# Performance work log

Hardware: AMD Instinct MI355X
Metric: run time of the kernel (lower is better)

## Reference

```python
import jax, jax.numpy as jnp
import numpy as np

B, S, H = 2, 2048, 3072
NH, NKV, HD = 16, 16, 256
Q_SIZE = NH * HD          # 4096
KV_SIZE = NKV * HD        # 4096
ROPE_THETA = 10000.0


def setup_inputs() -> dict:
    key = jax.random.key(0)
    k1, k2, k3 = jax.random.split(key, 3)
    hidden_states = jax.random.normal(k1, (B, S, H), dtype=jnp.float32)
    positions = jnp.arange(B * S, dtype=jnp.int32).reshape(B, S) % S  # 0..S-1 per row
    Wqkv = jax.random.normal(k2, (H, Q_SIZE + 2 * KV_SIZE), dtype=jnp.float32) * 0.02
    Wo = jax.random.normal(k3, (Q_SIZE, H), dtype=jnp.float32) * 0.02
    return {"hidden_states": hidden_states, "positions": positions, "Wqkv": Wqkv, "Wo": Wo}


def _apply_rope_neox(x, positions, head_dim, theta):
    # x: [B, S, nheads, head_dim]; neox style: rotate halves
    half = head_dim // 2
    inv_freq = 1.0 / (theta ** (jnp.arange(0, head_dim, 2, dtype=jnp.float32) / head_dim))  # [half]
    angles = positions.astype(jnp.float32)[..., None] * inv_freq  # [B, S, half]
    cos = jnp.cos(angles)[:, :, None, :]  # [B, S, 1, half]
    sin = jnp.sin(angles)[:, :, None, :]
    x1, x2 = x[..., :half], x[..., half:]
    return jnp.concatenate([x1 * cos - x2 * sin, x2 * cos + x1 * sin], axis=-1)


def reference(hidden_states, positions, Wqkv, Wo):
    # fused QKV projection (bias-free)
    qkv = jnp.einsum('bsh,hd->bsd', hidden_states, Wqkv)
    q, k, v = jnp.split(qkv, [Q_SIZE, Q_SIZE + KV_SIZE], axis=-1)
    q = q.reshape(B, S, NH, HD)
    k = k.reshape(B, S, NKV, HD)
    v = v.reshape(B, S, NKV, HD)
    # RoPE (neox style, rotary_dim == head_dim)
    q = _apply_rope_neox(q, positions, HD, ROPE_THETA)
    k = _apply_rope_neox(k, positions, HD, ROPE_THETA)
    # GQA: repeat kv heads if fewer than query heads
    if NKV != NH:
        rep = NH // NKV
        k = jnp.repeat(k, rep, axis=2)
        v = jnp.repeat(v, rep, axis=2)
    scale = float(HD) ** -0.5
    scores = jnp.einsum('bqhd,bkhd->bhqk', q, k) * scale  # [B, NH, S, S]
    causal = jnp.tril(jnp.ones((S, S), dtype=bool))
    scores = jnp.where(causal[None, None], scores, jnp.finfo(scores.dtype).min)
    probs = jax.nn.softmax(scores, axis=-1)
    attn = jnp.einsum('bhqk,bkhd->bqhd', probs, v).reshape(B, S, Q_SIZE)
    return jnp.einsum('bsd,dh->bsh', attn, Wo)
```

## Files before the change

### kernel.cpp

```cpp
#include <hip/hip_runtime.h>

#define SQLEN 2048
#define QKVW 12288
#define NHEADS 16
#define HEADD 256

typedef unsigned short u16;
typedef __bf16 bf16x8 __attribute__((ext_vector_type(8)));
typedef float f32x4 __attribute__((ext_vector_type(4)));

__device__ __forceinline__ float bf2f(u16 u) {
  union { unsigned int i; float f; } v; v.i = ((unsigned int)u) << 16; return v.f;
}
__device__ __forceinline__ u16 f2bf(float f) {
  union { float f; unsigned int i; } v; v.f = f;
  unsigned int x = v.i;
  return (u16)((x + 0x7fffu + ((x >> 16) & 1u)) >> 16);
}

__device__ __forceinline__ void gl_lds16(const u16* g, u16* l) {
  __builtin_amdgcn_global_load_lds(
      (const __attribute__((address_space(1))) void*)g,
      (__attribute__((address_space(3))) void*)l, 16, 0, 0);
}

__global__ __launch_bounds__(256) void f32_to_bf16(
    const float* __restrict__ src, u16* __restrict__ dst) {
  long i = (long)(blockIdx.x * 256 + threadIdx.x) * 8;
  float4 a = *reinterpret_cast<const float4*>(src + i);
  float4 b = *reinterpret_cast<const float4*>(src + i + 4);
  u16 tmp[8] = {f2bf(a.x), f2bf(a.y), f2bf(a.z), f2bf(a.w),
                f2bf(b.x), f2bf(b.y), f2bf(b.z), f2bf(b.w)};
  *reinterpret_cast<uint4*>(dst + i) = *reinterpret_cast<uint4*>(tmp);
}

__global__ __launch_bounds__(256) void ktranspose_f32(
    const float* __restrict__ src, u16* __restrict__ dst,
    int src_ld, int dst_ld) {
  __shared__ __align__(16) u16 t[64][64];
  const int c0 = blockIdx.x * 64, r0 = blockIdx.y * 64;
  const int tid = threadIdx.x;
  #pragma unroll
  for (int it = 0; it < 2; ++it) {
    int c = tid + it * 256;
    int r = c >> 3, ch = c & 7;
    const float* sp = src + (long)(r0 + r) * src_ld + c0 + ch * 8;
    float4 v0 = *reinterpret_cast<const float4*>(sp);
    float4 v1 = *reinterpret_cast<const float4*>(sp + 4);
    u16 tmp[8] = {f2bf(v0.x), f2bf(v0.y), f2bf(v0.z), f2bf(v0.w),
                  f2bf(v1.x), f2bf(v1.y), f2bf(v1.z), f2bf(v1.w)};
    int sw = ch ^ (r & 7);
    *reinterpret_cast<uint4*>(&t[r][sw * 8]) = *reinterpret_cast<uint4*>(tmp);
  }
  __syncthreads();
  #pragma unroll
  for (int it = 0; it < 2; ++it) {
    int c = tid + it * 256;
    int rr = c >> 3, ch = c & 7;
    u16 tmp[8];
    #pragma unroll
    for (int j = 0; j < 8; ++j) {
      int k = ch * 8 + j;
      int sw = (rr >> 3) ^ (k & 7);
      tmp[j] = t[k][sw * 8 + (rr & 7)];
    }
    *reinterpret_cast<uint4*>(dst + (long)(c0 + rr) * dst_ld + r0 + ch * 8) =
        *reinterpret_cast<uint4*>(tmp);
  }
}

__global__ __launch_bounds__(256) void ktranspose_bf16(
    const u16* __restrict__ src, u16* __restrict__ dst,
    int src_ld, int dst_ld, long src_off,
    long szs1, long szs2, long dzs1, long dzs2) {
  __shared__ __align__(16) u16 t[64][64];
  const int z = blockIdx.z;
  const u16* s = src + src_off + (long)(z >> 4) * szs1 + (long)(z & 15) * szs2;
  u16* d = dst + (long)(z >> 4) * dzs1 + (long)(z & 15) * dzs2;
  const int c0 = blockIdx.x * 64, r0 = blockIdx.y * 64;
  const int tid = threadIdx.x;
  #pragma unroll
  for (int it = 0; it < 2; ++it) {
    int c = tid + it * 256;
    int r = c >> 3, ch = c & 7;
    uint4 v = *reinterpret_cast<const uint4*>(s + (long)(r0 + r) * src_ld + c0 + ch * 8);
    int sw = ch ^ (r & 7);
    *reinterpret_cast<uint4*>(&t[r][sw * 8]) = v;
  }
  __syncthreads();
  #pragma unroll
  for (int it = 0; it < 2; ++it) {
    int c = tid + it * 256;
    int rr = c >> 3, ch = c & 7;
    u16 tmp[8];
    #pragma unroll
    for (int j = 0; j < 8; ++j) {
      int k = ch * 8 + j;
      int sw = (rr >> 3) ^ (k & 7);
      tmp[j] = t[k][sw * 8 + (rr & 7)];
    }
    *reinterpret_cast<uint4*>(d + (long)(c0 + rr) * dst_ld + r0 + ch * 8) =
        *reinterpret_cast<uint4*>(tmp);
  }
}

template <typename OUT_T>
__global__ __launch_bounds__(512, 2) void gemm_bt8(
    const u16* __restrict__ A, const u16* __restrict__ BT, OUT_T* __restrict__ C,
    int M, int N, int K) {
  (void)M;
  __shared__ __align__(16) u16 As[2][256][64];
  __shared__ __align__(16) u16 Bs[2][256][64];
  const int tid = threadIdx.x;
  const int wave = tid >> 6, lane = tid & 63;
  const int quad = lane >> 4, l16 = lane & 15;
  const int wm = (wave >> 2) * 128, wn = (wave & 3) * 64;
  const long m0 = (long)blockIdx.y * 256, n0 = (long)blockIdx.x * 256;
  const int sw = l16 & 7;
  const int ca0 = (quad ^ sw) * 8;
  const int ca1 = ((4 + quad) ^ sw) * 8;
  const int srow = tid >> 3;
  const int sdst8 = (tid & 7) * 8;
  const int ssrc8 = ((tid & 7) ^ (srow & 7)) * 8;
  const long Kl = K;
  const u16* gA = A + (m0 + srow) * Kl + ssrc8;
  const u16* gB = BT + (n0 + srow) * Kl + ssrc8;
  const int nt = K >> 6;

  f32x4 acc[8][4] = {};
  bf16x8 af[4][2];
  bf16x8 bfr[4][2];

#define STAGE_A(BB, R, K0) \
  gl_lds16(gA + (long)((R) << 6) * Kl + (K0), &As[BB][((R) << 6) + srow][sdst8])
#define STAGE_B(BB, R, K0) \
  gl_lds16(gB + (long)((R) << 6) * Kl + (K0), &Bs[BB][((R) << 6) + srow][sdst8])
#define READ_A(BB, RBASE)                                              \
  _Pragma("unroll") for (int i4 = 0; i4 < 4; ++i4) {                   \
    const u16* p_ = &As[BB][(RBASE) + i4 * 16 + l16][0];               \
    af[i4][0] = *reinterpret_cast<const bf16x8*>(p_ + ca0);            \
    af[i4][1] = *reinterpret_cast<const bf16x8*>(p_ + ca1);            \
  }
#define READ_B(BB, JB)                                                 \
  _Pragma("unroll") for (int j2 = 0; j2 < 2; ++j2) {                   \
    const u16* p_ = &Bs[BB][wn + ((JB) + j2) * 16 + l16][0];           \
    bfr[(JB) + j2][0] = *reinterpret_cast<const bf16x8*>(p_ + ca0);    \
    bfr[(JB) + j2][1] = *reinterpret_cast<const bf16x8*>(p_ + ca1);    \
  }
#define QUADMFMA(MB, NB)                                               \
  _Pragma("unroll") for (int i4 = 0; i4 < 4; ++i4)                     \
  _Pragma("unroll") for (int j2 = 0; j2 < 2; ++j2)                     \
  _Pragma("unroll") for (int s = 0; s < 2; ++s)                        \
    acc[(MB) + i4][(NB) + j2] = __builtin_amdgcn_mfma_f32_16x16x32_bf16( \
        af[i4][s], bfr[(NB) + j2][s], acc[(MB) + i4][(NB) + j2], 0, 0, 0);
#define BAR() asm volatile("s_barrier" ::: "memory")
#define LGKM0() asm volatile("s_waitcnt lgkmcnt(0)" ::: "memory")

  STAGE_A(0, 0, 0); STAGE_A(0, 1, 0); STAGE_A(0, 2, 0); STAGE_A(0, 3, 0);
  STAGE_B(0, 0, 0); STAGE_B(0, 1, 0); STAGE_B(0, 2, 0); STAGE_B(0, 3, 0);
  STAGE_A(1, 0, 64); STAGE_A(1, 1, 64);
  asm volatile("s_waitcnt vmcnt(2)" ::: "memory");
  BAR();

  for (int t = 0; t < nt; ++t) {
    const int b = t & 1;
    const long kn = (long)(t + 1) << 6;
    const long kn2 = (long)(t + 2) << 6;
    const bool st1 = (t + 1 < nt), st2 = (t + 2 < nt);
    READ_A(b, wm);
    READ_B(b, 0);
    if (st1) { STAGE_A(b ^ 1, 2, kn); STAGE_A(b ^ 1, 3, kn); }
    BAR(); LGKM0();
    __builtin_amdgcn_s_setprio(1);
    QUADMFMA(0, 0);
    __builtin_amdgcn_s_setprio(0);
    BAR();
    READ_B(b, 2);
    if (st1) { STAGE_B(b ^ 1, 0, kn); STAGE_B(b ^ 1, 1, kn); }
    BAR(); LGKM0();
    __builtin_amdgcn_s_setprio(1);
    QUADMFMA(0, 2);
    __builtin_amdgcn_s_setprio(0);
    BAR();
    READ_A(b, wm + 64);
    if (st1) { STAGE_B(b ^ 1, 2, kn); STAGE_B(b ^ 1, 3, kn); }
    BAR(); LGKM0();
    __builtin_amdgcn_s_setprio(1);
    QUADMFMA(4, 2);
    __builtin_amdgcn_s_setprio(0);
    BAR();
    if (st2) { STAGE_A(b, 0, kn2); STAGE_A(b, 1, kn2); }
    BAR();
    __builtin_amdgcn_s_setprio(1);
    QUADMFMA(4, 0);
    __builtin_amdgcn_s_setprio(0);
    if (st2) asm volatile("s_waitcnt vmcnt(2)" ::: "memory");
    else     asm volatile("s_waitcnt vmcnt(0)" ::: "memory");
    BAR();
  }

  #pragma unroll
  for (int i = 0; i < 8; ++i)
    #pragma unroll
    for (int j = 0; j < 4; ++j) {
      long col = n0 + wn + j * 16 + l16;
      #pragma unroll
      for (int r = 0; r < 4; ++r) {
        long row = m0 + wm + i * 16 + quad * 4 + r;
        if constexpr (sizeof(OUT_T) == 4)
          C[row * (long)N + col] = acc[i][j][r];
        else
          C[row * (long)N + col] = f2bf(acc[i][j][r]);
      }
    }
#undef STAGE_A
#undef STAGE_B
#undef READ_A
#undef READ_B
#undef QUADMFMA
#undef BAR
#undef LGKM0
}

__global__ __launch_bounds__(256) void rope_kernel(
    u16* __restrict__ qkv, const int* __restrict__ positions) {
  int idx = blockIdx.x * 256 + threadIdx.x;
  int i = idx & 127;
  int head = (idx >> 7) & 31;
  int row = idx >> 12;
  int col = (head < NHEADS) ? head * HEADD : 4096 + (head - NHEADS) * HEADD;
  u16* p = qkv + (long)row * QKVW + col;
  float x1 = bf2f(p[i]), x2 = bf2f(p[i + 128]);
  float pos = (float)positions[row];
  float inv_freq = exp2f((float)i * (-13.287712379549449f / 128.0f));
  float ang = pos * inv_freq;
  float sv, cv;
  sincosf(ang, &sv, &cv);
  p[i] = f2bf(x1 * cv - x2 * sv);
  p[i + 128] = f2bf(x2 * cv + x1 * sv);
}

__global__ __launch_bounds__(256, 1) void attn_kernel(
    const u16* __restrict__ qkv, const u16* __restrict__ VT,
    u16* __restrict__ attnout) {
  const int p = blockIdx.x;
  const int bh = blockIdx.y;
  const int b = bh >> 4, h = bh & 15;
  const int tid = threadIdx.x;
  const int wave = tid >> 6, lane = tid & 63;
  const int quad = lane >> 4, l16 = lane & 15;

  __shared__ __align__(16) u16 Ks[64][264];
  __shared__ __align__(16) u16 Vs[256][72];
  __shared__ __align__(16) u16 Ps[64][72];

  const u16* qp = qkv + (long)b * SQLEN * QKVW + h * HEADD;
  const u16* kp = qp + 4096;
  const u16* vtp = VT + (long)bh * HEADD * SQLEN;
  const float cs = 0.0625f * 1.4426950408889634f;

  for (int half = 0; half < 2; ++half) {
    const int qt = half ? p : 31 - p;

    #pragma unroll
    for (int it = 0; it < 8; ++it) {
      int c = tid + it * 256;
      int r = c >> 5, c8 = (c & 31) * 8;
      *reinterpret_cast<uint4*>(&Ks[r][c8]) =
          *reinterpret_cast<const uint4*>(qp + (long)(qt * 64 + r) * QKVW + c8);
    }
    __syncthreads();
    bf16x8 qf[8];
    #pragma unroll
    for (int s = 0; s < 8; ++s)
      qf[s] = *reinterpret_cast<const bf16x8*>(&Ks[wave * 16 + l16][s * 32 + quad * 8]);
    __syncthreads();

    float m_i[4], l_i[4];
    #pragma unroll
    for (int r = 0; r < 4; ++r) { m_i[r] = -INFINITY; l_i[r] = 0.f; }
    f32x4 o[16] = {};

    for (int kt = 0; kt <= qt; ++kt) {
      #pragma unroll
      for (int it = 0; it < 8; ++it) {
        int c = tid + it * 256;
        int r = c >> 5, c8 = (c & 31) * 8;
        *reinterpret_cast<uint4*>(&Ks[r][c8]) =
            *reinterpret_cast<const uint4*>(kp + (long)(kt * 64 + r) * QKVW + c8);
      }
      #pragma unroll
      for (int it = 0; it < 8; ++it) {
        int c = tid + it * 256;
        int r = c >> 3, c8 = (c & 7) * 8;
        *reinterpret_cast<uint4*>(&Vs[r][c8]) =
            *reinterpret_cast<const uint4*>(vtp + (long)r * SQLEN + kt * 64 + c8);
      }
      __syncthreads();

      f32x4 sc[4] = {};
      #pragma unroll
      for (int s = 0; s < 8; ++s) {
        #pragma unroll
        for (int nb = 0; nb < 4; ++nb) {
          bf16x8 kf = *reinterpret_cast<const bf16x8*>(&Ks[nb * 16 + l16][s * 32 + quad * 8]);
          sc[nb] = __builtin_amdgcn_mfma_f32_16x16x32_bf16(qf[s], kf, sc[nb], 0, 0, 0);
        }
      }
      const bool diag = (kt == qt);
      #pragma unroll
      for (int nb = 0; nb < 4; ++nb)
        #pragma unroll
        for (int r = 0; r < 4; ++r) {
          float v = sc[nb][r] * cs;
          if (diag) {
            int colL = nb * 16 + l16, rowL = wave * 16 + quad * 4 + r;
            if (colL > rowL) v = -INFINITY;
          }
          sc[nb][r] = v;
        }
      float alpha[4];
      #pragma unroll
      for (int r = 0; r < 4; ++r) {
        float t = fmaxf(fmaxf(sc[0][r], sc[1][r]), fmaxf(sc[2][r], sc[3][r]));
        #pragma unroll
        for (int d = 1; d < 16; d <<= 1) t = fmaxf(t, __shfl_xor(t, d));
        float mn = fmaxf(m_i[r], t);
        alpha[r] = exp2f(m_i[r] - mn);
        m_i[r] = mn;
      }
      #pragma unroll
      for (int r = 0; r < 4; ++r) {
        float t = 0.f;
        #pragma unroll
        for (int nb = 0; nb < 4; ++nb) {
          float pr = exp2f(sc[nb][r] - m_i[r]);
          sc[nb][r] = pr;
          t += pr;
        }
        #pragma unroll
        for (int d = 1; d < 16; d <<= 1) t += __shfl_xor(t, d);
        l_i[r] = l_i[r] * alpha[r] + t;
      }
      #pragma unroll
      for (int nb = 0; nb < 4; ++nb)
        #pragma unroll
        for (int r = 0; r < 4; ++r)
          Ps[wave * 16 + quad * 4 + r][nb * 16 + l16] = f2bf(sc[nb][r]);
      #pragma unroll
      for (int c16 = 0; c16 < 16; ++c16)
        #pragma unroll
        for (int r = 0; r < 4; ++r)
          o[c16][r] *= alpha[r];
      __syncthreads();
      bf16x8 pf[2];
      #pragma unroll
      for (int s2 = 0; s2 < 2; ++s2)
        pf[s2] = *reinterpret_cast<const bf16x8*>(&Ps[wave * 16 + l16][s2 * 32 + quad * 8]);
      #pragma unroll
      for (int c16 = 0; c16 < 16; ++c16) {
        #pragma unroll
        for (int s2 = 0; s2 < 2; ++s2) {
          bf16x8 vf = *reinterpret_cast<const bf16x8*>(&Vs[c16 * 16 + l16][s2 * 32 + quad * 8]);
          o[c16] = __builtin_amdgcn_mfma_f32_16x16x32_bf16(pf[s2], vf, o[c16], 0, 0, 0);
        }
      }
      __syncthreads();
    }
    #pragma unroll
    for (int r = 0; r < 4; ++r) {
      float inv = 1.0f / l_i[r];
      long q = qt * 64 + wave * 16 + quad * 4 + r;
      long rowoff = ((long)b * SQLEN + q) * 4096 + h * HEADD;
      #pragma unroll
      for (int c16 = 0; c16 < 16; ++c16)
        attnout[rowoff + c16 * 16 + l16] = f2bf(o[c16][r] * inv);
    }
  }
}

extern "C" void kernel_launch(void* const* d_in, const int* in_sizes, int n_in,
                              void* d_out, int out_size, void* d_ws, size_t ws_size,
                              hipStream_t stream) {
  const float* hidden = (const float*)d_in[0];
  const int* positions = (const int*)d_in[1];
  const float* Wqkv = (const float*)d_in[2];
  const float* Wo = (const float*)d_in[3];
  float* out = (float*)d_out;
  char* ws = (char*)d_ws;

  u16* qkv     = (u16*)(ws);
  u16* WqkvT   = (u16*)(ws + 100663296L);
  u16* attn    = (u16*)(ws + 100663296L);
  u16* WoT     = (u16*)(ws + 134217728L);
  u16* hiddenB = (u16*)(ws + 176160768L);
  u16* VT      = (u16*)(ws + 176160768L);

  f32_to_bf16<<<dim3(6144, 1, 1), 256, 0, stream>>>(hidden, hiddenB);
  ktranspose_f32<<<dim3(192, 48, 1), 256, 0, stream>>>(Wqkv, WqkvT, 12288, 3072);
  gemm_bt8<u16><<<dim3(48, 16, 1), 512, 0, stream>>>(
      hiddenB, WqkvT, qkv, 4096, 12288, 3072);
  rope_kernel<<<dim3(65536, 1, 1), 256, 0, stream>>>(qkv, positions);
  ktranspose_bf16<<<dim3(4, 32, 32), 256, 0, stream>>>(
      qkv, VT, 12288, 2048, 8192,
      25165824L, 256L, 8388608L, 524288L);
  attn_kernel<<<dim3(16, 32, 1), 256, 0, stream>>>(qkv, VT, attn);
  ktranspose_f32<<<dim3(48, 64, 1), 256, 0, stream>>>(Wo, WoT, 3072, 4096);
  gemm_bt8<float><<<dim3(12, 16, 1), 512, 0, stream>>>(
      attn, WoT, out, 4096, 3072, 4096);
}
```

Before: 967.7 us.

## Double-buffer attention K/V via direct LDS loads and deepen GEMM prefetch

The attention kernel now stages K and V tiles into double-buffered, XOR-swizzled LDS with global_load_lds, prefetching two tiles ahead. Q is loaded straight from global memory into registers, and the MFMA sections are wrapped in setprio. The GEMM reorders its staging so a full next stage is in flight before the loop, waits on vmcnt(6), and remaps blocks so consecutive tiles share an XCD for cache locality. Together these aim to hide global-load latency behind MFMA work. In exchange they double LDS use in attention, which may limit occupancy, and bring fragile hand-tuned waitcnt and barrier ordering.

```diff
diff --git a/kernel.cpp b/kernel.cpp
--- a/kernel.cpp
+++ b/kernel.cpp
@@ -115,7 +115,11 @@
   const int wave = tid >> 6, lane = tid & 63;
   const int quad = lane >> 4, l16 = lane & 15;
   const int wm = (wave >> 2) * 128, wn = (wave & 3) * 64;
-  const long m0 = (long)blockIdx.y * 256, n0 = (long)blockIdx.x * 256;
+  const int gx = gridDim.x;
+  const int flat = blockIdx.y * gx + blockIdx.x;
+  const int cpx = (gx * gridDim.y) >> 3;
+  const int virt = (flat & 7) * cpx + (flat >> 3);
+  const long m0 = (long)(virt / gx) * 256, n0 = (long)(virt % gx) * 256;
   const int sw = l16 & 7;
   const int ca0 = (quad ^ sw) * 8;
   const int ca1 = ((4 + quad) ^ sw) * 8;
@@ -158,8 +162,14 @@
 
   STAGE_A(0, 0, 0); STAGE_A(0, 1, 0); STAGE_A(0, 2, 0); STAGE_A(0, 3, 0);
   STAGE_B(0, 0, 0); STAGE_B(0, 1, 0); STAGE_B(0, 2, 0); STAGE_B(0, 3, 0);
-  STAGE_A(1, 0, 64); STAGE_A(1, 1, 64);
-  asm volatile("s_waitcnt vmcnt(2)" ::: "memory");
+  if (nt > 1) {
+    STAGE_A(1, 0, 64); STAGE_A(1, 2, 64);
+    STAGE_B(1, 0, 64); STAGE_B(1, 1, 64);
+    STAGE_A(1, 1, 64); STAGE_A(1, 3, 64);
+    asm volatile("s_waitcnt vmcnt(6)" ::: "memory");
+  } else {
+    asm volatile("s_waitcnt vmcnt(0)" ::: "memory");
+  }
   BAR();
 
   for (int t = 0; t < nt; ++t) {
@@ -169,33 +179,34 @@
     const bool st1 = (t + 1 < nt), st2 = (t + 2 < nt);
     READ_A(b, wm);
     READ_B(b, 0);
-    if (st1) { STAGE_A(b ^ 1, 2, kn); STAGE_A(b ^ 1, 3, kn); }
+    if (st1) { STAGE_B(b ^ 1, 2, kn); STAGE_B(b ^ 1, 3, kn); }
+    asm volatile("s_waitcnt lgkmcnt(8)" ::: "memory");
     BAR(); LGKM0();
     __builtin_amdgcn_s_setprio(1);
     QUADMFMA(0, 0);
     __builtin_amdgcn_s_setprio(0);
     BAR();
     READ_B(b, 2);
-    if (st1) { STAGE_B(b ^ 1, 0, kn); STAGE_B(b ^ 1, 1, kn); }
+    if (st2) { STAGE_A(b, 0, kn2); STAGE_A(b, 2, kn2); }
     BAR(); LGKM0();
     __builtin_amdgcn_s_setprio(1);
     QUADMFMA(0, 2);
     __builtin_amdgcn_s_setprio(0);
     BAR();
     READ_A(b, wm + 64);
-    if (st1) { STAGE_B(b ^ 1, 2, kn); STAGE_B(b ^ 1, 3, kn); }
+    if (st2) { STAGE_B(b, 0, kn2); STAGE_B(b, 1, kn2); }
     BAR(); LGKM0();
     __builtin_amdgcn_s_setprio(1);
     QUADMFMA(4, 2);
     __builtin_amdgcn_s_setprio(0);
     BAR();
-    if (st2) { STAGE_A(b, 0, kn2); STAGE_A(b, 1, kn2); }
+    if (st2) { STAGE_A(b, 1, kn2); STAGE_A(b, 3, kn2); }
     BAR();
     __builtin_amdgcn_s_setprio(1);
     QUADMFMA(4, 0);
     __builtin_amdgcn_s_setprio(0);
-    if (st2) asm volatile("s_waitcnt vmcnt(2)" ::: "memory");
-    else     asm volatile("s_waitcnt vmcnt(0)" ::: "memory");
+    if (st2)      asm volatile("s_waitcnt vmcnt(6)" ::: "memory");
+    else if (st1) asm volatile("s_waitcnt vmcnt(0)" ::: "memory");
     BAR();
   }
 
@@ -243,15 +254,18 @@
 __global__ __launch_bounds__(256, 1) void attn_kernel(
     const u16* __restrict__ qkv, const u16* __restrict__ VT,
     u16* __restrict__ attnout) {
-  const int p = blockIdx.x;
-  const int bh = blockIdx.y;
+  const int s_hw = blockIdx.y * 16 + blockIdx.x;
+  const int xcd = s_hw & 7, idx = s_hw >> 3;
+  const int bh = xcd * 4 + (idx >> 4);
+  const int p = idx & 15;
   const int b = bh >> 4, h = bh & 15;
   const int tid = threadIdx.x;
   const int wave = tid >> 6, lane = tid & 63;
   const int quad = lane >> 4, l16 = lane & 15;
-
-  __shared__ __align__(16) u16 Ks[64][264];
-  __shared__ __align__(16) u16 Vs[256][72];
+  const int sw7 = l16 & 7;
+
+  __shared__ __align__(16) u16 Ks[2][64][256];
+  __shared__ __align__(16) u16 Vs[2][256][64];
   __shared__ __align__(16) u16 Ps[64][72];
 
   const u16* qp = qkv + (long)b * SQLEN * QKVW + h * HEADD;
@@ -259,22 +273,37 @@
   const u16* vtp = VT + (long)bh * HEADD * SQLEN;
   const float cs = 0.0625f * 1.4426950408889634f;
 
+  const u16* ksrc = kp + (long)(tid >> 5) * QKVW + ((tid & 31) ^ ((tid >> 5) & 7)) * 8;
+  const u16* vsrc = vtp + (long)(tid >> 3) * SQLEN + ((tid & 7) ^ ((tid >> 3) & 7)) * 8;
+  u16* kdst = &Ks[0][0][0] + tid * 8;
+  u16* vdst = &Vs[0][0][0] + tid * 8;
+
+#define STAGE_K(KT, BB) { const u16* gk_ = ksrc + (long)(KT) * 64 * QKVW;      \
+  _Pragma("unroll") for (int it = 0; it < 8; ++it)                             \
+    gl_lds16(gk_ + (long)it * 8 * QKVW, kdst + (BB) * 16384 + it * 2048); }
+#define STAGE_V(KT, BB) { const u16* gv_ = vsrc + (KT) * 64;                   \
+  _Pragma("unroll") for (int it = 0; it < 8; ++it)                             \
+    gl_lds16(gv_ + (long)it * 32 * SQLEN, vdst + (BB) * 16384 + it * 2048); }
+#define ABAR() asm volatile("s_barrier" ::: "memory")
+
   for (int half = 0; half < 2; ++half) {
     const int qt = half ? p : 31 - p;
 
-    #pragma unroll
-    for (int it = 0; it < 8; ++it) {
-      int c = tid + it * 256;
-      int r = c >> 5, c8 = (c & 31) * 8;
-      *reinterpret_cast<uint4*>(&Ks[r][c8]) =
-          *reinterpret_cast<const uint4*>(qp + (long)(qt * 64 + r) * QKVW + c8);
-    }
-    __syncthreads();
+    ABAR();
+    const u16* qrow = qp + (long)(qt * 64 + wave * 16 + l16) * QKVW + quad * 8;
     bf16x8 qf[8];
     #pragma unroll
     for (int s = 0; s < 8; ++s)
-      qf[s] = *reinterpret_cast<const bf16x8*>(&Ks[wave * 16 + l16][s * 32 + quad * 8]);
-    __syncthreads();
+      qf[s] = *reinterpret_cast<const bf16x8*>(qrow + s * 32);
+
+    STAGE_K(0, 0); STAGE_V(0, 0);
+    if (qt > 0) {
+      STAGE_K(1, 1); STAGE_V(1, 1);
+      asm volatile("s_waitcnt vmcnt(16)" ::: "memory");
+    } else {
+      asm volatile("s_waitcnt vmcnt(0)" ::: "memory");
+    }
+    ABAR();
 
     float m_i[4], l_i[4];
     #pragma unroll
@@ -282,31 +311,19 @@
     f32x4 o[16] = {};
 
     for (int kt = 0; kt <= qt; ++kt) {
-      #pragma unroll
-      for (int it = 0; it < 8; ++it) {
-        int c = tid + it * 256;
-        int r = c >> 5, c8 = (c & 31) * 8;
-        *reinterpret_cast<uint4*>(&Ks[r][c8]) =
-            *reinterpret_cast<const uint4*>(kp + (long)(kt * 64 + r) * QKVW + c8);
-      }
-      #pragma unroll
-      for (int it = 0; it < 8; ++it) {
-        int c = tid + it * 256;
-        int r = c >> 3, c8 = (c & 7) * 8;
-        *reinterpret_cast<uint4*>(&Vs[r][c8]) =
-            *reinterpret_cast<const uint4*>(vtp + (long)r * SQLEN + kt * 64 + c8);
-      }
-      __syncthreads();
-
+      const int bb = kt & 1;
       f32x4 sc[4] = {};
+      __builtin_amdgcn_s_setprio(1);
       #pragma unroll
       for (int s = 0; s < 8; ++s) {
         #pragma unroll
         for (int nb = 0; nb < 4; ++nb) {
-          bf16x8 kf = *reinterpret_cast<const bf16x8*>(&Ks[nb * 16 + l16][s * 32 + quad * 8]);
+          bf16x8 kf = *reinterpret_cast<const bf16x8*>(
+              &Ks[bb][nb * 16 + l16][(((s << 2) + quad) ^ sw7) * 8]);
           sc[nb] = __builtin_amdgcn_mfma_f32_16x16x32_bf16(qf[s], kf, sc[nb], 0, 0, 0);
         }
       }
+      __builtin_amdgcn_s_setprio(0);
       const bool diag = (kt == qt);
       #pragma unroll
       for (int nb = 0; nb < 4; ++nb)
@@ -342,6 +359,8 @@
         for (int d = 1; d < 16; d <<= 1) t += __shfl_xor(t, d);
         l_i[r] = l_i[r] * alpha[r] + t;
       }
+      ABAR();
+      if (kt + 2 <= qt) STAGE_K(kt + 2, bb);
       #pragma unroll
       for (int nb = 0; nb < 4; ++nb)
         #pragma unroll
@@ -352,20 +371,31 @@
         #pragma unroll
         for (int r = 0; r < 4; ++r)
           o[c16][r] *= alpha[r];
-      __syncthreads();
       bf16x8 pf[2];
       #pragma unroll
       for (int s2 = 0; s2 < 2; ++s2)
         pf[s2] = *reinterpret_cast<const bf16x8*>(&Ps[wave * 16 + l16][s2 * 32 + quad * 8]);
+      __builtin_amdgcn_s_setprio(1);
       #pragma unroll
       for (int c16 = 0; c16 < 16; ++c16) {
         #pragma unroll
         for (int s2 = 0; s2 < 2; ++s2) {
-          bf16x8 vf = *reinterpret_cast<const bf16x8*>(&Vs[c16 * 16 + l16][s2 * 32 + quad * 8]);
+          bf16x8 vf = *reinterpret_cast<const bf16x8*>(
+              &Vs[bb][c16 * 16 + l16][(((s2 << 2) + quad) ^ sw7) * 8]);
           o[c16] = __builtin_amdgcn_mfma_f32_16x16x32_bf16(pf[s2], vf, o[c16], 0, 0, 0);
         }
       }
-      __syncthreads();
+      __builtin_amdgcn_s_setprio(0);
+      if (kt < qt) {
+        ABAR();
+        if (kt + 2 <= qt) {
+          STAGE_V(kt + 2, bb);
+          asm volatile("s_waitcnt vmcnt(16)" ::: "memory");
+        } else {
+          asm volatile("s_waitcnt vmcnt(0)" ::: "memory");
+        }
+        ABAR();
+      }
     }
     #pragma unroll
     for (int r = 0; r < 4; ++r) {
@@ -377,6 +407,9 @@
         attnout[rowoff + c16 * 16 + l16] = f2bf(o[c16][r] * inv);
     }
   }
+#undef STAGE_K
+#undef STAGE_V
+#undef ABAR
 }
 
 extern "C" void kernel_launch(void* const* d_in, const int* in_sizes, int n_in,
```

After: 996.9 us. +3.0%, slower.
